# Optimization experiments

Hardware: AMD Instinct MI355X
Metric: run time of the kernel (lower is better)

Reference implementation:

```python
import jax, jax.numpy as jnp
import numpy as np


def setup_inputs() -> dict:
    key = jax.random.key(0)
    kq, kk, kv = jax.random.split(key, 3)
    B, H, S, D = 4, 16, 1024, 64
    Q = jax.random.normal(kq, (B, H, S, D), dtype=jnp.float32)
    K = jax.random.normal(kk, (B, H, S, D), dtype=jnp.float32)
    V = jax.random.normal(kv, (B, H, S, D), dtype=jnp.float32)
    attn_mask = jnp.ones((B, 1, 1, S), dtype=jnp.int32)  # unused by the original forward
    return {"Q": Q, "K": K, "V": V, "attn_mask": attn_mask, "d_k": D}


def reference(Q, K, V, attn_mask, d_k):
    # scores = Q @ K^T / sqrt(d_k)   -> [B, H, S, S]
    scores = jnp.einsum("bhqd,bhkd->bhqk", Q, K) / jnp.sqrt(jnp.float32(d_k))
    # attn_mask is accepted but never applied in the original module.
    p_attn = jax.nn.softmax(scores, axis=-1)
    out = jnp.einsum("bhqk,bhkd->bhqd", p_attn, V)  # [B, H, S, D]
    return (out, p_attn)
```

## Files before the change

### kernel.cpp

```cpp
#include <hip/hip_runtime.h>
#include <hip/hip_bf16.h>

#define B_N 4
#define H_N 16
#define S_N 1024
#define D_N 64
#define NELEM (B_N * H_N * S_N * D_N)

typedef __bf16 bf16;
typedef bf16  bf16x4 __attribute__((ext_vector_type(4)));
typedef bf16  bf16x8 __attribute__((ext_vector_type(8)));
typedef float f32x4  __attribute__((ext_vector_type(4)));
typedef unsigned int u32x2 __attribute__((ext_vector_type(2)));

#define AS1 __attribute__((address_space(1)))
#define AS3 __attribute__((address_space(3)))
#define GLL16(gp, lp) __builtin_amdgcn_global_load_lds((const AS1 void*)(gp), (AS3 void*)(lp), 16, 0, 0)

__global__ __launch_bounds__(256)
void prep_kv(const float* __restrict__ K, const float* __restrict__ V,
             bf16* __restrict__ Kb, bf16* __restrict__ Vt)
{
    const int b = blockIdx.x;
    if (b < 2048) {
        int t = b * 256 + threadIdx.x;
        int row = t >> 3, sub = t & 7;
        const float* src = K + (size_t)row * 64 + sub * 8;
        float4 f0 = *(const float4*)src;
        float4 f1 = *(const float4*)(src + 4);
        bf16x8 o;
        o[0] = (bf16)f0.x; o[1] = (bf16)f0.y; o[2] = (bf16)f0.z; o[3] = (bf16)f0.w;
        o[4] = (bf16)f1.x; o[5] = (bf16)f1.y; o[6] = (bf16)f1.z; o[7] = (bf16)f1.w;
        int slot = sub ^ (row & 7);
        *(bf16x8*)(Kb + (size_t)row * 64 + slot * 8) = o;
    } else {
        int wid  = (b - 2048) * 4 + (threadIdx.x >> 6);
        int lane = threadIdx.x & 63;
        int bh = wid >> 7, chunk = wid & 127;
        const float* src = V + (size_t)bh * S_N * D_N + (size_t)chunk * 8 * 64 + lane;
        bf16x8 o;
#pragma unroll
        for (int j = 0; j < 8; ++j) o[j] = (bf16)src[j * 64];
        int slot = (chunk & 7) ^ (lane & 7);
        bf16* dst = Vt + (size_t)bh * D_N * S_N + (size_t)lane * S_N
                       + (chunk >> 3) * 64 + slot * 8;
        *(bf16x8*)dst = o;
    }
}

__global__ __launch_bounds__(256)
void sdpa_main(const float* __restrict__ Qf, const bf16* __restrict__ Kb,
               const bf16* __restrict__ Vt, float* __restrict__ Og,
               float* __restrict__ Pg)
{
    __shared__ __attribute__((aligned(128))) bf16 K_lds[2][4096];
    __shared__ __attribute__((aligned(128))) bf16 V_lds[2][4096];
    __shared__ __attribute__((aligned(128))) bf16 Pt_lds[4][1024];

    const int bid = blockIdx.x;
    const int swz = (bid & 7) * 128 + (bid >> 3);
    const int bh = swz >> 4, qtile = swz & 15;

    const int tid = threadIdx.x;
    const int wave = tid >> 6, lane = tid & 63;
    const int l16 = lane & 15, lgrp = lane >> 4;
    const int swx = (l16 & 7) << 4;

    const float* Qp = Qf + (size_t)bh * S_N * D_N;
    const bf16* Kp = Kb + (size_t)bh * S_N * D_N;
    const bf16* Vp = Vt + (size_t)bh * D_N * S_N;
    float* Op = Og + (size_t)bh * S_N * D_N;
    float* Pp = Pg + (size_t)bh * S_N * S_N;

    const int qrow = qtile * 64 + wave * 16 + l16;
    bf16x8 aq[2];
#pragma unroll
    for (int ds = 0; ds < 2; ++ds) {
        const float* src = Qp + (size_t)qrow * 64 + ds * 32 + lgrp * 8;
        float4 f0 = *(const float4*)src;
        float4 f1 = *(const float4*)(src + 4);
        aq[ds][0] = (bf16)(f0.x * 0.125f); aq[ds][1] = (bf16)(f0.y * 0.125f);
        aq[ds][2] = (bf16)(f0.z * 0.125f); aq[ds][3] = (bf16)(f0.w * 0.125f);
        aq[ds][4] = (bf16)(f1.x * 0.125f); aq[ds][5] = (bf16)(f1.y * 0.125f);
        aq[ds][6] = (bf16)(f1.z * 0.125f); aq[ds][7] = (bf16)(f1.w * 0.125f);
    }

    auto stage_k = [&](int kt, bf16* dst) {
        const bf16* gk = Kp + (size_t)kt * 64;
        GLL16(gk + (wave    ) * 512 + lane * 8, dst + (wave    ) * 512);
        GLL16(gk + (wave + 4) * 512 + lane * 8, dst + (wave + 4) * 512);
    };
    auto stage_k2 = [&](int kt, bf16* dst0, bf16* dst1) {
        const bf16* gk = Kp + (size_t)kt * 64;
        GLL16(gk + (wave     ) * 512 + lane * 8, dst0 + (wave    ) * 512);
        GLL16(gk + (wave + 4 ) * 512 + lane * 8, dst0 + (wave + 4) * 512);
        GLL16(gk + (wave + 8 ) * 512 + lane * 8, dst1 + (wave    ) * 512);
        GLL16(gk + (wave + 12) * 512 + lane * 8, dst1 + (wave + 4) * 512);
    };
    auto stage_v = [&](int kt, bf16* dst) {
        const int dr = lane >> 3, c7 = lane & 7;
        GLL16(Vp + (size_t)((wave    ) * 8 + dr) * S_N + kt + c7 * 8, dst + (wave    ) * 512);
        GLL16(Vp + (size_t)((wave + 4) * 8 + dr) * S_N + kt + c7 * 8, dst + (wave + 4) * 512);
    };

    auto scores = [&](const bf16* base, f32x4 (&acc)[4]) {
#pragma unroll
        for (int kb = 0; kb < 4; ++kb) {
            acc[kb] = (f32x4){0.f, 0.f, 0.f, 0.f};
#pragma unroll
            for (int ds = 0; ds < 2; ++ds) {
                bf16x8 bk = *(const bf16x8*)((const char*)base
                            + (kb * 16 + l16) * 128
                            + ((ds * 64 + lgrp * 16) ^ swx));
                acc[kb] = __builtin_amdgcn_mfma_f32_16x16x32_bf16(aq[ds], bk, acc[kb], 0, 0, 0);
            }
        }
    };

    float lsum[4] = {0.f, 0.f, 0.f, 0.f};
    stage_k2(0, &K_lds[0][0], &K_lds[1][0]);
    __syncthreads();
    for (int c = 0; c < 8; ++c) {
        const bf16* b0 = (c & 1) ? &V_lds[0][0] : &K_lds[0][0];
        const bf16* b1 = (c & 1) ? &V_lds[1][0] : &K_lds[1][0];
        bf16* n0 = (c & 1) ? &K_lds[0][0] : &V_lds[0][0];
        bf16* n1 = (c & 1) ? &K_lds[1][0] : &V_lds[1][0];
        if (c < 7) stage_k2((c + 1) * 128, n0, n1);
        f32x4 acc[4];
        scores(b0, acc);
#pragma unroll
        for (int kb = 0; kb < 4; ++kb)
#pragma unroll
            for (int r = 0; r < 4; ++r) lsum[r] += __expf(acc[kb][r]);
        scores(b1, acc);
#pragma unroll
        for (int kb = 0; kb < 4; ++kb)
#pragma unroll
            for (int r = 0; r < 4; ++r) lsum[r] += __expf(acc[kb][r]);
        __syncthreads();
    }
    float rl[4];
#pragma unroll
    for (int r = 0; r < 4; ++r) {
        float s = lsum[r];
        s += __shfl_xor(s, 1, 64);
        s += __shfl_xor(s, 2, 64);
        s += __shfl_xor(s, 4, 64);
        s += __shfl_xor(s, 8, 64);
        rl[r] = 1.0f / s;
    }

    f32x4 oacc[4];
#pragma unroll
    for (int db = 0; db < 4; ++db) oacc[db] = (f32x4){0.f, 0.f, 0.f, 0.f};

    const unsigned ptoff = (unsigned)(uintptr_t)(AS3 bf16*)(&Pt_lds[wave][0]);
    const int qg = qtile * 64 + wave * 16 + l16;

    stage_k(0, &K_lds[0][0]);
    stage_v(0, &V_lds[0][0]);
    asm volatile("s_waitcnt vmcnt(0)" ::: "memory");
    __builtin_amdgcn_s_barrier();
    for (int t = 0; t < 16; ++t) {
        const int kt = t * 64, buf = t & 1;

        f32x4 acc[4];
        scores(&K_lds[buf][0], acc);

        if (t < 15) {
            stage_k(kt + 64, &K_lds[buf ^ 1][0]);
            stage_v(kt + 64, &V_lds[buf ^ 1][0]);
        }

#pragma unroll
        for (int kb = 0; kb < 4; ++kb) {
            bf16x4 pk;
#pragma unroll
            for (int r = 0; r < 4; ++r) pk[r] = (bf16)(__expf(acc[kb][r]) * rl[r]);
            *(bf16x4*)((char*)&Pt_lds[wave][0] + (kb * 16 + l16) * 32 + lgrp * 8) = pk;
        }
        asm volatile("s_waitcnt lgkmcnt(0)" ::: "memory");

        const bf16* vb = &V_lds[buf][0];
#pragma unroll
        for (int ks = 0; ks < 2; ++ks) {
            bf16x8 bv0 = *(const bf16x8*)((const char*)vb + (l16     ) * 128 + ((ks * 64 + lgrp * 16) ^ swx));
            bf16x8 bv1 = *(const bf16x8*)((const char*)vb + (16 + l16) * 128 + ((ks * 64 + lgrp * 16) ^ swx));
            bf16x8 bv2 = *(const bf16x8*)((const char*)vb + (32 + l16) * 128 + ((ks * 64 + lgrp * 16) ^ swx));
            bf16x8 bv3 = *(const bf16x8*)((const char*)vb + (48 + l16) * 128 + ((ks * 64 + lgrp * 16) ^ swx));

            u32x2 t0, t1;
            unsigned a = ptoff + ks * 1024 + lgrp * 256 + l16 * 8;
            asm volatile("ds_read_b64_tr_b16 %0, %2\n\t"
                         "ds_read_b64_tr_b16 %1, %2 offset:128"
                         : "=&v"(t0), "=&v"(t1) : "v"(a));
            asm volatile("s_waitcnt lgkmcnt(0)" ::: "memory");
            __builtin_amdgcn_sched_barrier(0);

            bf16x8 ap;
            ((unsigned*)&ap)[0] = t0[0]; ((unsigned*)&ap)[1] = t0[1];
            ((unsigned*)&ap)[2] = t1[0]; ((unsigned*)&ap)[3] = t1[1];

            float4 o0, o1;
            o0.x = __uint_as_float(t0[0] << 16);
            o0.y = __uint_as_float(t0[0] & 0xffff0000u);
            o0.z = __uint_as_float(t0[1] << 16);
            o0.w = __uint_as_float(t0[1] & 0xffff0000u);
            o1.x = __uint_as_float(t1[0] << 16);
            o1.y = __uint_as_float(t1[0] & 0xffff0000u);
            o1.z = __uint_as_float(t1[1] << 16);
            o1.w = __uint_as_float(t1[1] & 0xffff0000u);
            float* pp = Pp + (size_t)qg * S_N + kt + ks * 32 + lgrp * 8;
            *(float4*)pp = o0;
            *(float4*)(pp + 4) = o1;

            oacc[0] = __builtin_amdgcn_mfma_f32_16x16x32_bf16(ap, bv0, oacc[0], 0, 0, 0);
            oacc[1] = __builtin_amdgcn_mfma_f32_16x16x32_bf16(ap, bv1, oacc[1], 0, 0, 0);
            oacc[2] = __builtin_amdgcn_mfma_f32_16x16x32_bf16(ap, bv2, oacc[2], 0, 0, 0);
            oacc[3] = __builtin_amdgcn_mfma_f32_16x16x32_bf16(ap, bv3, oacc[3], 0, 0, 0);
        }

        asm volatile("s_waitcnt vmcnt(8)" ::: "memory");
        __builtin_amdgcn_s_barrier();
    }

    const int qb0 = qtile * 64 + wave * 16 + lgrp * 4;
#pragma unroll
    for (int db = 0; db < 4; ++db)
#pragma unroll
        for (int r = 0; r < 4; ++r)
            Op[(size_t)(qb0 + r) * D_N + db * 16 + l16] = oacc[db][r];
}

__global__ __launch_bounds__(256)
void sdpa_fused(const float* __restrict__ Qg, const float* __restrict__ Kg,
                const float* __restrict__ Vg, float* __restrict__ Og,
                float* __restrict__ Pg)
{
    constexpr int LDP = 72;
    __shared__ bf16 K_lds [64][LDP];
    __shared__ bf16 Vt_lds[64][LDP];
    __shared__ bf16 P_lds [4][16][LDP];

    const int qtile = blockIdx.x;
    const int bh    = blockIdx.y;
    const int tid   = threadIdx.x;
    const int wave  = tid >> 6;
    const int lane  = tid & 63;
    const int l16   = lane & 15;
    const int lgrp  = lane >> 4;

    const float* Qp = Qg + (size_t)bh * S_N * D_N;
    const float* Kp = Kg + (size_t)bh * S_N * D_N;
    const float* Vp = Vg + (size_t)bh * S_N * D_N;
    float* Op = Og + (size_t)bh * S_N * D_N;
    float* Pp = Pg + (size_t)bh * S_N * S_N;

    const int qrow = qtile * 64 + wave * 16 + l16;
    bf16x8 aq[2];
#pragma unroll
    for (int ds = 0; ds < 2; ++ds) {
        const float* src = Qp + qrow * D_N + ds * 32 + lgrp * 8;
        float4 f0 = *(const float4*)(src);
        float4 f1 = *(const float4*)(src + 4);
        aq[ds][0] = (bf16)(f0.x * 0.125f); aq[ds][1] = (bf16)(f0.y * 0.125f);
        aq[ds][2] = (bf16)(f0.z * 0.125f); aq[ds][3] = (bf16)(f0.w * 0.125f);
        aq[ds][4] = (bf16)(f1.x * 0.125f); aq[ds][5] = (bf16)(f1.y * 0.125f);
        aq[ds][6] = (bf16)(f1.z * 0.125f); aq[ds][7] = (bf16)(f1.w * 0.125f);
    }

    auto stage_k = [&](int kt) {
#pragma unroll
        for (int i = 0; i < 4; ++i) {
            int slot = tid + i * 256;
            int row = slot >> 4, c4 = slot & 15;
            float4 f = *(const float4*)(Kp + (kt + row) * D_N + c4 * 4);
            bf16x4 pk = {(bf16)f.x, (bf16)f.y, (bf16)f.z, (bf16)f.w};
            *(bf16x4*)&K_lds[row][c4 * 4] = pk;
        }
    };
    auto stage_v = [&](int kt) {
#pragma unroll
        for (int i = 0; i < 4; ++i) {
            int slot = tid + i * 256;
            int row = slot >> 4, c4 = slot & 15;
            float4 f = *(const float4*)(Vp + (kt + row) * D_N + c4 * 4);
            Vt_lds[c4 * 4 + 0][row] = (bf16)f.x;
            Vt_lds[c4 * 4 + 1][row] = (bf16)f.y;
            Vt_lds[c4 * 4 + 2][row] = (bf16)f.z;
            Vt_lds[c4 * 4 + 3][row] = (bf16)f.w;
        }
    };
    auto compute_scores = [&](f32x4 (&acc)[4]) {
#pragma unroll
        for (int kb = 0; kb < 4; ++kb) {
            acc[kb] = (f32x4){0.f, 0.f, 0.f, 0.f};
#pragma unroll
            for (int ds = 0; ds < 2; ++ds) {
                bf16x8 bk = *(const bf16x8*)&K_lds[kb * 16 + l16][ds * 32 + lgrp * 8];
                acc[kb] = __builtin_amdgcn_mfma_f32_16x16x32_bf16(aq[ds], bk, acc[kb], 0, 0, 0);
            }
        }
    };

    float lsum[4] = {0.f, 0.f, 0.f, 0.f};
    for (int kt = 0; kt < S_N; kt += 64) {
        __syncthreads();
        stage_k(kt);
        __syncthreads();
        f32x4 acc[4];
        compute_scores(acc);
#pragma unroll
        for (int kb = 0; kb < 4; ++kb)
#pragma unroll
            for (int r = 0; r < 4; ++r) lsum[r] += __expf(acc[kb][r]);
    }
    float rl[4];
#pragma unroll
    for (int r = 0; r < 4; ++r) {
        float s = lsum[r];
        s += __shfl_xor(s, 1, 64);
        s += __shfl_xor(s, 2, 64);
        s += __shfl_xor(s, 4, 64);
        s += __shfl_xor(s, 8, 64);
        rl[r] = 1.0f / s;
    }

    f32x4 oacc[4];
#pragma unroll
    for (int db = 0; db < 4; ++db) oacc[db] = (f32x4){0.f, 0.f, 0.f, 0.f};
    const int qb0 = qtile * 64 + wave * 16 + lgrp * 4;

    for (int kt = 0; kt < S_N; kt += 64) {
        __syncthreads();
        stage_k(kt);
        stage_v(kt);
        __syncthreads();

        f32x4 acc[4];
        compute_scores(acc);
#pragma unroll
        for (int kb = 0; kb < 4; ++kb) {
#pragma unroll
            for (int r = 0; r < 4; ++r) {
                float p = __expf(acc[kb][r]) * rl[r];
                Pp[(size_t)(qb0 + r) * S_N + (kt + kb * 16 + l16)] = p;
                P_lds[wave][lgrp * 4 + r][kb * 16 + l16] = (bf16)p;
            }
        }
#pragma unroll
        for (int ks = 0; ks < 2; ++ks) {
            bf16x8 ap = *(const bf16x8*)&P_lds[wave][l16][ks * 32 + lgrp * 8];
#pragma unroll
            for (int db = 0; db < 4; ++db) {
                bf16x8 bv = *(const bf16x8*)&Vt_lds[db * 16 + l16][ks * 32 + lgrp * 8];
                oacc[db] = __builtin_amdgcn_mfma_f32_16x16x32_bf16(ap, bv, oacc[db], 0, 0, 0);
            }
        }
    }

#pragma unroll
    for (int db = 0; db < 4; ++db)
#pragma unroll
        for (int r = 0; r < 4; ++r)
            Op[(size_t)(qb0 + r) * D_N + db * 16 + l16] = oacc[db][r];
}

extern "C" void kernel_launch(void* const* d_in, const int* in_sizes, int n_in,
                              void* d_out, int out_size, void* d_ws, size_t ws_size,
                              hipStream_t stream) {
    const float* Q = (const float*)d_in[0];
    const float* K = (const float*)d_in[1];
    const float* V = (const float*)d_in[2];
    float* Out = (float*)d_out;
    float* P   = (float*)d_out + (size_t)NELEM;

    const size_t need = (size_t)NELEM * 2 * 2;
    if (ws_size >= need) {
        bf16* Kb = (bf16*)d_ws;
        bf16* Vt = Kb + NELEM;
        prep_kv<<<dim3(4096), dim3(256), 0, stream>>>(K, V, Kb, Vt);
        sdpa_main<<<dim3(1024), dim3(256), 0, stream>>>(Q, Kb, Vt, Out, P);
    } else {
        sdpa_fused<<<dim3(16, 64), dim3(256), 0, stream>>>(Q, K, V, Out, P);
    }
}
```

Before: 96.87 us.

## Halve query and key tiles to 32 rows with 2-wave blocks

The main SDPA kernel now processes 32 query rows per block with 128 threads (2 waves) and walks keys in 32-wide tiles, launching 2048 blocks instead of 1024. The V transpose layout in prep_kv changes to a 32-column swizzle to match the narrower key tile, and the LDS buffers shrink. The goal is more blocks and smaller LDS per block for better occupancy and latency hiding. In exchange each K/V tile is reused by fewer query rows, so global K/V traffic doubles, and there are twice as many barriers per pass.

```diff
diff --git a/kernel.cpp b/kernel.cpp
--- a/kernel.cpp
+++ b/kernel.cpp
@@ -41,25 +41,25 @@
         bf16x8 o;
 #pragma unroll
         for (int j = 0; j < 8; ++j) o[j] = (bf16)src[j * 64];
-        int slot = (chunk & 7) ^ (lane & 7);
+        int s = (chunk & 3) ^ ((lane >> 1) & 3);
         bf16* dst = Vt + (size_t)bh * D_N * S_N + (size_t)lane * S_N
-                       + (chunk >> 3) * 64 + slot * 8;
+                       + (chunk >> 2) * 32 + s * 8;
         *(bf16x8*)dst = o;
     }
 }
 
-__global__ __launch_bounds__(256)
+__global__ __launch_bounds__(128)
 void sdpa_main(const float* __restrict__ Qf, const bf16* __restrict__ Kb,
                const bf16* __restrict__ Vt, float* __restrict__ Og,
                float* __restrict__ Pg)
 {
-    __shared__ __attribute__((aligned(128))) bf16 K_lds[2][4096];
-    __shared__ __attribute__((aligned(128))) bf16 V_lds[2][4096];
-    __shared__ __attribute__((aligned(128))) bf16 Pt_lds[4][1024];
+    __shared__ __attribute__((aligned(128))) bf16 K_lds[2][2048];
+    __shared__ __attribute__((aligned(128))) bf16 V_lds[2][2048];
+    __shared__ __attribute__((aligned(128))) bf16 Pt_lds[2][512];
 
     const int bid = blockIdx.x;
-    const int swz = (bid & 7) * 128 + (bid >> 3);
-    const int bh = swz >> 4, qtile = swz & 15;
+    const int swz = (bid & 7) * 256 + (bid >> 3);
+    const int bh = swz >> 5, qtile = swz & 31;
 
     const int tid = threadIdx.x;
     const int wave = tid >> 6, lane = tid & 63;
@@ -72,7 +72,7 @@
     float* Op = Og + (size_t)bh * S_N * D_N;
     float* Pp = Pg + (size_t)bh * S_N * S_N;
 
-    const int qrow = qtile * 64 + wave * 16 + l16;
+    const int qrow = qtile * 32 + wave * 16 + l16;
     bf16x8 aq[2];
 #pragma unroll
     for (int ds = 0; ds < 2; ++ds) {
@@ -88,24 +88,17 @@
     auto stage_k = [&](int kt, bf16* dst) {
         const bf16* gk = Kp + (size_t)kt * 64;
         GLL16(gk + (wave    ) * 512 + lane * 8, dst + (wave    ) * 512);
-        GLL16(gk + (wave + 4) * 512 + lane * 8, dst + (wave + 4) * 512);
-    };
-    auto stage_k2 = [&](int kt, bf16* dst0, bf16* dst1) {
-        const bf16* gk = Kp + (size_t)kt * 64;
-        GLL16(gk + (wave     ) * 512 + lane * 8, dst0 + (wave    ) * 512);
-        GLL16(gk + (wave + 4 ) * 512 + lane * 8, dst0 + (wave + 4) * 512);
-        GLL16(gk + (wave + 8 ) * 512 + lane * 8, dst1 + (wave    ) * 512);
-        GLL16(gk + (wave + 12) * 512 + lane * 8, dst1 + (wave + 4) * 512);
+        GLL16(gk + (wave + 2) * 512 + lane * 8, dst + (wave + 2) * 512);
     };
     auto stage_v = [&](int kt, bf16* dst) {
-        const int dr = lane >> 3, c7 = lane & 7;
-        GLL16(Vp + (size_t)((wave    ) * 8 + dr) * S_N + kt + c7 * 8, dst + (wave    ) * 512);
-        GLL16(Vp + (size_t)((wave + 4) * 8 + dr) * S_N + kt + c7 * 8, dst + (wave + 4) * 512);
-    };
-
-    auto scores = [&](const bf16* base, f32x4 (&acc)[4]) {
-#pragma unroll
-        for (int kb = 0; kb < 4; ++kb) {
+        const int dr = lane >> 2, c = lane & 3;
+        GLL16(Vp + (size_t)(wave * 16 + dr     ) * S_N + kt + c * 8, dst + wave * 512);
+        GLL16(Vp + (size_t)(wave * 16 + dr + 32) * S_N + kt + c * 8, dst + 1024 + wave * 512);
+    };
+
+    auto scores = [&](const bf16* base, f32x4 (&acc)[2]) {
+#pragma unroll
+        for (int kb = 0; kb < 2; ++kb) {
             acc[kb] = (f32x4){0.f, 0.f, 0.f, 0.f};
 #pragma unroll
             for (int ds = 0; ds < 2; ++ds) {
@@ -118,23 +111,24 @@
     };
 
     float lsum[4] = {0.f, 0.f, 0.f, 0.f};
-    stage_k2(0, &K_lds[0][0], &K_lds[1][0]);
+    stage_k(0, &K_lds[0][0]);
+    stage_k(32, &K_lds[1][0]);
     __syncthreads();
-    for (int c = 0; c < 8; ++c) {
+    for (int c = 0; c < 16; ++c) {
         const bf16* b0 = (c & 1) ? &V_lds[0][0] : &K_lds[0][0];
         const bf16* b1 = (c & 1) ? &V_lds[1][0] : &K_lds[1][0];
         bf16* n0 = (c & 1) ? &K_lds[0][0] : &V_lds[0][0];
         bf16* n1 = (c & 1) ? &K_lds[1][0] : &V_lds[1][0];
-        if (c < 7) stage_k2((c + 1) * 128, n0, n1);
-        f32x4 acc[4];
+        if (c < 15) { stage_k((c + 1) * 64, n0); stage_k((c + 1) * 64 + 32, n1); }
+        f32x4 acc[2];
         scores(b0, acc);
 #pragma unroll
-        for (int kb = 0; kb < 4; ++kb)
+        for (int kb = 0; kb < 2; ++kb)
 #pragma unroll
             for (int r = 0; r < 4; ++r) lsum[r] += __expf(acc[kb][r]);
         scores(b1, acc);
 #pragma unroll
-        for (int kb = 0; kb < 4; ++kb)
+        for (int kb = 0; kb < 2; ++kb)
 #pragma unroll
             for (int r = 0; r < 4; ++r) lsum[r] += __expf(acc[kb][r]);
         __syncthreads();
@@ -155,25 +149,25 @@
     for (int db = 0; db < 4; ++db) oacc[db] = (f32x4){0.f, 0.f, 0.f, 0.f};
 
     const unsigned ptoff = (unsigned)(uintptr_t)(AS3 bf16*)(&Pt_lds[wave][0]);
-    const int qg = qtile * 64 + wave * 16 + l16;
+    const int qg = qtile * 32 + wave * 16 + l16;
 
     stage_k(0, &K_lds[0][0]);
     stage_v(0, &V_lds[0][0]);
     asm volatile("s_waitcnt vmcnt(0)" ::: "memory");
     __builtin_amdgcn_s_barrier();
-    for (int t = 0; t < 16; ++t) {
-        const int kt = t * 64, buf = t & 1;
-
-        f32x4 acc[4];
+    for (int t = 0; t < 32; ++t) {
+        const int kt = t * 32, buf = t & 1;
+
+        f32x4 acc[2];
         scores(&K_lds[buf][0], acc);
 
-        if (t < 15) {
-            stage_k(kt + 64, &K_lds[buf ^ 1][0]);
-            stage_v(kt + 64, &V_lds[buf ^ 1][0]);
-        }
-
-#pragma unroll
-        for (int kb = 0; kb < 4; ++kb) {
+        if (t < 31) {
+            stage_k(kt + 32, &K_lds[buf ^ 1][0]);
+            stage_v(kt + 32, &V_lds[buf ^ 1][0]);
+        }
+
+#pragma unroll
+        for (int kb = 0; kb < 2; ++kb) {
             bf16x4 pk;
 #pragma unroll
             for (int r = 0; r < 4; ++r) pk[r] = (bf16)(__expf(acc[kb][r]) * rl[r]);
@@ -182,49 +176,50 @@
         asm volatile("s_waitcnt lgkmcnt(0)" ::: "memory");
 
         const bf16* vb = &V_lds[buf][0];
-#pragma unroll
-        for (int ks = 0; ks < 2; ++ks) {
-            bf16x8 bv0 = *(const bf16x8*)((const char*)vb + (l16     ) * 128 + ((ks * 64 + lgrp * 16) ^ swx));
-            bf16x8 bv1 = *(const bf16x8*)((const char*)vb + (16 + l16) * 128 + ((ks * 64 + lgrp * 16) ^ swx));
-            bf16x8 bv2 = *(const bf16x8*)((const char*)vb + (32 + l16) * 128 + ((ks * 64 + lgrp * 16) ^ swx));
-            bf16x8 bv3 = *(const bf16x8*)((const char*)vb + (48 + l16) * 128 + ((ks * 64 + lgrp * 16) ^ swx));
-
-            u32x2 t0, t1;
-            unsigned a = ptoff + ks * 1024 + lgrp * 256 + l16 * 8;
-            asm volatile("ds_read_b64_tr_b16 %0, %2\n\t"
-                         "ds_read_b64_tr_b16 %1, %2 offset:128"
-                         : "=&v"(t0), "=&v"(t1) : "v"(a));
-            asm volatile("s_waitcnt lgkmcnt(0)" ::: "memory");
-            __builtin_amdgcn_sched_barrier(0);
-
-            bf16x8 ap;
-            ((unsigned*)&ap)[0] = t0[0]; ((unsigned*)&ap)[1] = t0[1];
-            ((unsigned*)&ap)[2] = t1[0]; ((unsigned*)&ap)[3] = t1[1];
-
-            float4 o0, o1;
-            o0.x = __uint_as_float(t0[0] << 16);
-            o0.y = __uint_as_float(t0[0] & 0xffff0000u);
-            o0.z = __uint_as_float(t0[1] << 16);
-            o0.w = __uint_as_float(t0[1] & 0xffff0000u);
-            o1.x = __uint_as_float(t1[0] << 16);
-            o1.y = __uint_as_float(t1[0] & 0xffff0000u);
-            o1.z = __uint_as_float(t1[1] << 16);
-            o1.w = __uint_as_float(t1[1] & 0xffff0000u);
-            float* pp = Pp + (size_t)qg * S_N + kt + ks * 32 + lgrp * 8;
-            *(float4*)pp = o0;
-            *(float4*)(pp + 4) = o1;
-
-            oacc[0] = __builtin_amdgcn_mfma_f32_16x16x32_bf16(ap, bv0, oacc[0], 0, 0, 0);
-            oacc[1] = __builtin_amdgcn_mfma_f32_16x16x32_bf16(ap, bv1, oacc[1], 0, 0, 0);
-            oacc[2] = __builtin_amdgcn_mfma_f32_16x16x32_bf16(ap, bv2, oacc[2], 0, 0, 0);
-            oacc[3] = __builtin_amdgcn_mfma_f32_16x16x32_bf16(ap, bv3, oacc[3], 0, 0, 0);
-        }
-
-        asm volatile("s_waitcnt vmcnt(8)" ::: "memory");
+        bf16x8 bv0, bv1, bv2, bv3;
+        {
+            const int vsw = ((l16 >> 1) & 3) << 4;
+            bv0 = *(const bf16x8*)((const char*)vb + (l16     ) * 64 + ((lgrp * 16) ^ vsw));
+            bv1 = *(const bf16x8*)((const char*)vb + (16 + l16) * 64 + ((lgrp * 16) ^ vsw));
+            bv2 = *(const bf16x8*)((const char*)vb + (32 + l16) * 64 + ((lgrp * 16) ^ vsw));
+            bv3 = *(const bf16x8*)((const char*)vb + (48 + l16) * 64 + ((lgrp * 16) ^ vsw));
+        }
+
+        u32x2 t0, t1;
+        unsigned a = ptoff + lgrp * 256 + l16 * 8;
+        asm volatile("ds_read_b64_tr_b16 %0, %2\n\t"
+                     "ds_read_b64_tr_b16 %1, %2 offset:128"
+                     : "=&v"(t0), "=&v"(t1) : "v"(a));
+        asm volatile("s_waitcnt lgkmcnt(0)" ::: "memory");
+        __builtin_amdgcn_sched_barrier(0);
+
+        bf16x8 ap;
+        ((unsigned*)&ap)[0] = t0[0]; ((unsigned*)&ap)[1] = t0[1];
+        ((unsigned*)&ap)[2] = t1[0]; ((unsigned*)&ap)[3] = t1[1];
+
+        float4 o0, o1;
+        o0.x = __uint_as_float(t0[0] << 16);
+        o0.y = __uint_as_float(t0[0] & 0xffff0000u);
+        o0.z = __uint_as_float(t0[1] << 16);
+        o0.w = __uint_as_float(t0[1] & 0xffff0000u);
+        o1.x = __uint_as_float(t1[0] << 16);
+        o1.y = __uint_as_float(t1[0] & 0xffff0000u);
+        o1.z = __uint_as_float(t1[1] << 16);
+        o1.w = __uint_as_float(t1[1] & 0xffff0000u);
+        float* pp = Pp + (size_t)qg * S_N + kt + lgrp * 8;
+        *(float4*)pp = o0;
+        *(float4*)(pp + 4) = o1;
+
+        oacc[0] = __builtin_amdgcn_mfma_f32_16x16x32_bf16(ap, bv0, oacc[0], 0, 0, 0);
+        oacc[1] = __builtin_amdgcn_mfma_f32_16x16x32_bf16(ap, bv1, oacc[1], 0, 0, 0);
+        oacc[2] = __builtin_amdgcn_mfma_f32_16x16x32_bf16(ap, bv2, oacc[2], 0, 0, 0);
+        oacc[3] = __builtin_amdgcn_mfma_f32_16x16x32_bf16(ap, bv3, oacc[3], 0, 0, 0);
+
+        asm volatile("s_waitcnt vmcnt(2)" ::: "memory");
         __builtin_amdgcn_s_barrier();
     }
 
-    const int qb0 = qtile * 64 + wave * 16 + lgrp * 4;
+    const int qb0 = qtile * 32 + wave * 16 + lgrp * 4;
 #pragma unroll
     for (int db = 0; db < 4; ++db)
 #pragma unroll
@@ -380,7 +375,7 @@
         bf16* Kb = (bf16*)d_ws;
         bf16* Vt = Kb + NELEM;
         prep_kv<<<dim3(4096), dim3(256), 0, stream>>>(K, V, Kb, Vt);
-        sdpa_main<<<dim3(1024), dim3(256), 0, stream>>>(Q, Kb, Vt, Out, P);
+        sdpa_main<<<dim3(2048), dim3(128), 0, stream>>>(Q, Kb, Vt, Out, P);
     } else {
         sdpa_fused<<<dim3(16, 64), dim3(256), 0, stream>>>(Q, K, V, Out, P);
     }
```

Result: slower. 110.2 us (+13.8%).
